# Optimization experiments

Hardware: AMD Instinct MI355X
Metric: run time of the kernel (lower is better)

## Reference

```python
import jax, jax.numpy as jnp
import numpy as np

B, N, K = 2, 1024, 32
NUM_RBF = 16
NUM_POS = 16
EDGE_C = 128
MAXREL = 32
# atoms15 = [N, CA, C, O, virtual-CB, SC0..SC9]; 25 bb-bb pairs + 40 bb-sidechain pairs
_bb = np.arange(5)
SRC = np.concatenate([np.repeat(_bb, 5), np.repeat(np.arange(4), 10)])  # (65,)
DST = np.concatenate([np.tile(_bb, 5), np.tile(np.arange(5, 15), 4)])   # (65,)
P = 65
EDGE_IN = NUM_POS + NUM_RBF * P + 1  # 1057


def setup_inputs() -> dict:
    key = jax.random.key(0)
    ks = jax.random.split(key, 12)
    return {
        "atom14_coords": jax.random.normal(ks[0], (B, N, 14, 3), jnp.float32),
        "atom14_cond_mask": jnp.ones((B, N, 14), jnp.float32),
        "noise": jax.random.normal(ks[1], (B, N, 14, 3), jnp.float32),
        "residue_index": jnp.arange(B * N, dtype=jnp.int32).reshape(B, N),
        "asym_id": jax.random.randint(ks[2], (B, N), 0, 4, jnp.int32),
        "token_bonds": jax.random.uniform(ks[3], (B, N, N), jnp.float32),
        "is_ligand": jax.random.bernoulli(ks[4], 0.2, (B, N)),
        "pos_W": jax.random.normal(ks[5], (2 * MAXREL + 2, NUM_POS), jnp.float32) * 0.1,
        "pos_b": jax.random.normal(ks[6], (NUM_POS,), jnp.float32) * 0.1,
        "edge_W": jax.random.normal(ks[7], (EDGE_IN, EDGE_C), jnp.float32) * 0.02,
        "ln_gamma": jnp.ones((EDGE_C,), jnp.float32),
        "ln_beta": jnp.zeros((EDGE_C,), jnp.float32),
    }


def _gather_nodes(x, idx):
    # x: [B,N,...], idx: [B,N,K] -> [B,N,K,...]
    return jax.vmap(lambda a, i: a[i])(x, idx)


def _rbf(D):
    # D: [...,] -> [..., NUM_RBF]
    D_mu = jnp.linspace(2.0, 22.0, NUM_RBF)
    D_sigma = (22.0 - 2.0) / NUM_RBF
    return jnp.exp(-(((D[..., None] - D_mu) / D_sigma) ** 2))


def reference(atom14_coords, atom14_cond_mask, noise, residue_index, asym_id,
              token_bonds, is_ligand, pos_W, pos_b, edge_W, ln_gamma, ln_beta):
    X = atom14_coords + noise
    X = jnp.where(atom14_cond_mask[..., None] > 0, X, X[..., 1:2, :])
    CA = X[..., 1, :]                                  # [B,N,3]
    mask = atom14_cond_mask[..., 1]                    # [B,N]

    # --- KNN on CA distances ---
    mask_2D = mask[:, None, :] * mask[:, :, None]      # [B,N,N]
    dX = CA[:, None, :, :] - CA[:, :, None, :]
    D = mask_2D * jnp.sqrt(jnp.sum(dX * dX, -1) + 1e-6)
    D_max = jnp.max(D, -1, keepdims=True)
    D_adjust = D + (1.0 - mask_2D) * D_max
    neg_vals, E_idx = jax.lax.top_k(-D_adjust, K)      # smallest K, ascending
    D_neighbors = -neg_vals                            # [B,N,K]

    # --- virtual CB and 15-atom set ---
    b = X[:, :, 1, :] - X[:, :, 0, :]
    c = X[:, :, 2, :] - X[:, :, 1, :]
    a = jnp.cross(b, c)
    Cb = -0.58273431 * a + 0.56802827 * b - 0.54067466 * c + X[:, :, 1, :]
    atoms15 = jnp.concatenate([X[:, :, :4, :], Cb[:, :, None, :], X[:, :, 4:14, :]], axis=2)  # [B,N,15,3]

    # --- fused gather + pairwise distances + RBF over 65 atom pairs ---
    nb_atoms = _gather_nodes(atoms15, E_idx)           # [B,N,K,15,3]
    A = atoms15[:, :, SRC, :]                          # [B,N,65,3]
    Bn = nb_atoms[:, :, :, DST, :]                     # [B,N,K,65,3]
    diff = A[:, :, None, :, :] - Bn
    D_pairs = jnp.sqrt(jnp.sum(diff * diff, -1) + 1e-6)   # [B,N,K,65]
    RBF_all = _rbf(D_pairs).reshape(B, N, K, P * NUM_RBF)  # [B,N,K,1040]

    # --- positional encodings ---
    offset = residue_index[:, :, None] - residue_index[:, None, :]
    offset_nb = jnp.take_along_axis(offset, E_idx, axis=2)     # [B,N,K]
    chain_labels = asym_id  # use_multichain_encoding=True
    d_chains = (chain_labels[:, :, None] == chain_labels[:, None, :]).astype(jnp.int32)
    E_chains = jnp.take_along_axis(d_chains, E_idx, axis=2)    # [B,N,K]
    d = jnp.clip(offset_nb + MAXREL, 0, 2 * MAXREL) * E_chains + (1 - E_chains) * (2 * MAXREL + 1)
    d_onehot = jax.nn.one_hot(d, 2 * MAXREL + 2, dtype=jnp.float32)
    E_positional = d_onehot @ pos_W + pos_b                    # [B,N,K,16]

    # --- token bonds ---
    tb_mask = jnp.logical_or(is_ligand[:, :, None], is_ligand[:, None, :])
    tb = token_bonds * tb_mask.astype(token_bonds.dtype)
    tb_nb = jnp.take_along_axis(tb, E_idx, axis=2)[..., None]  # [B,N,K,1]

    # --- edge embedding + layernorm ---
    E = jnp.concatenate([E_positional, RBF_all, tb_nb], axis=-1)  # [B,N,K,1057]
    E = E @ edge_W                                                # [B,N,K,128]
    mu = jnp.mean(E, -1, keepdims=True)
    var = jnp.mean((E - mu) ** 2, -1, keepdims=True)
    E = (E - mu) / jnp.sqrt(var + 1e-5) * ln_gamma + ln_beta
    return (E, E_idx, D_neighbors)
```

## Files before the change

### kernel.cpp

```cpp
#include <hip/hip_runtime.h>
#include <math.h>

#define BB 2
#define NN 1024
#define KNN 32
#define PP 65
#define NRBF 16
#define EC 128
#define KPAD 1088
#define NCHUNK 17
#define NKT 34

typedef __attribute__((ext_vector_type(8))) short bf16x8;
typedef __attribute__((ext_vector_type(4))) float f32x4;

__device__ __forceinline__ ushort f2bf(float f) {
    union { float f; unsigned u; } v; v.f = f;
    unsigned r = v.u + 0x7fffu + ((v.u >> 16) & 1u);
    return (ushort)(r >> 16);
}

__global__ __launch_bounds__(256) void k_atoms(
    const float* __restrict__ coords, const float* __restrict__ mask,
    const float* __restrict__ noise, float* __restrict__ atoms15)
{
    int idx = blockIdx.x * blockDim.x + threadIdx.x;
    if (idx >= BB * NN) return;
    const float* c  = coords + (size_t)idx * 42;
    const float* nz = noise  + (size_t)idx * 42;
    const float* m  = mask   + (size_t)idx * 14;

    float X[14][3];
    float x1[3];
#pragma unroll
    for (int d = 0; d < 3; d++) x1[d] = c[3 + d] + nz[3 + d];
#pragma unroll
    for (int a = 0; a < 14; a++) {
        bool mm = m[a] > 0.0f;
#pragma unroll
        for (int d = 0; d < 3; d++) {
            float v = c[a * 3 + d] + nz[a * 3 + d];
            X[a][d] = mm ? v : x1[d];
        }
    }
    float bv[3], cv[3], av[3], cb[3];
#pragma unroll
    for (int d = 0; d < 3; d++) { bv[d] = X[1][d] - X[0][d]; cv[d] = X[2][d] - X[1][d]; }
    av[0] = bv[1] * cv[2] - bv[2] * cv[1];
    av[1] = bv[2] * cv[0] - bv[0] * cv[2];
    av[2] = bv[0] * cv[1] - bv[1] * cv[0];
#pragma unroll
    for (int d = 0; d < 3; d++)
        cb[d] = -0.58273431f * av[d] + 0.56802827f * bv[d] - 0.54067466f * cv[d] + X[1][d];

    float* o = atoms15 + (size_t)idx * 45;
#pragma unroll
    for (int a = 0; a < 4; a++)
#pragma unroll
        for (int d = 0; d < 3; d++) o[a * 3 + d] = X[a][d];
#pragma unroll
    for (int d = 0; d < 3; d++) o[4 * 3 + d] = cb[d];
#pragma unroll
    for (int a = 0; a < 10; a++)
#pragma unroll
        for (int d = 0; d < 3; d++) o[(5 + a) * 3 + d] = X[4 + a][d];
}

__global__ __launch_bounds__(256) void k_knn(
    const float* __restrict__ atoms15, const float* __restrict__ cond,
    float* __restrict__ out_idx_f, float* __restrict__ out_d, int* __restrict__ eidx)
{
    __shared__ float Dadj[NN];
    __shared__ float m2s[NN];
    __shared__ float rmax[4];
    __shared__ float candv[128];
    __shared__ int   candj[128];

    int row = blockIdx.x;
    int b = row >> 10, i = row & (NN - 1);
    int t = threadIdx.x;
    int ln = t & 63, wv = t >> 6;
    const float* ab = atoms15 + (size_t)b * NN * 45;
    float cax = ab[(size_t)i * 45 + 3];
    float cay = ab[(size_t)i * 45 + 4];
    float caz = ab[(size_t)i * 45 + 5];
    float mi = cond[(size_t)row * 14 + 1];

    float lmax = -1e30f;
    for (int j = t; j < NN; j += 256) {
        float dx = cax - ab[(size_t)j * 45 + 3];
        float dy = cay - ab[(size_t)j * 45 + 4];
        float dz = caz - ab[(size_t)j * 45 + 5];
        float mj = cond[((size_t)b * NN + j) * 14 + 1];
        float m2 = mi * mj;
        float D = m2 * sqrtf(dx * dx + dy * dy + dz * dz + 1e-6f);
        Dadj[j] = D; m2s[j] = m2;
        lmax = fmaxf(lmax, D);
    }
#pragma unroll
    for (int off = 32; off > 0; off >>= 1) lmax = fmaxf(lmax, __shfl_xor(lmax, off));
    if (ln == 0) rmax[wv] = lmax;
    __syncthreads();
    float Dmax = fmaxf(fmaxf(rmax[0], rmax[1]), fmaxf(rmax[2], rmax[3]));
    for (int j = t; j < NN; j += 256) Dadj[j] += (1.0f - m2s[j]) * Dmax;
    __syncthreads();

    const int base = wv * 256 + ln;
    float v0 = Dadj[base];
    float v1 = Dadj[base + 64];
    float v2 = Dadj[base + 128];
    float v3 = Dadj[base + 192];

    float selv = 0.0f; int seli = 0;
    for (int k = 0; k < KNN; k++) {
        float bv = v0; int bj = base;
        if (v1 < bv) { bv = v1; bj = base + 64;  }
        if (v2 < bv) { bv = v2; bj = base + 128; }
        if (v3 < bv) { bv = v3; bj = base + 192; }
#pragma unroll
        for (int off = 1; off < 64; off <<= 1) {
            float ov = __shfl_xor(bv, off);
            int   oj = __shfl_xor(bj, off);
            if (ov < bv || (ov == bv && oj < bj)) { bv = ov; bj = oj; }
        }
        if (ln == k) { selv = bv; seli = bj; }
        if (bj == base)            v0 = 1e30f;
        else if (bj == base + 64)  v1 = 1e30f;
        else if (bj == base + 128) v2 = 1e30f;
        else if (bj == base + 192) v3 = 1e30f;
    }
    if (ln < KNN) { candv[wv * KNN + ln] = selv; candj[wv * KNN + ln] = seli; }
    __syncthreads();

    if (wv == 0) {
        float c0v = candv[ln];      int c0j = candj[ln];
        float c1v = candv[64 + ln]; int c1j = candj[64 + ln];
        float fv = 0.0f; int fj = 0;
        for (int k = 0; k < KNN; k++) {
            float bv; int bj;
            if (c0v < c1v || (c0v == c1v && c0j < c1j)) { bv = c0v; bj = c0j; }
            else                                        { bv = c1v; bj = c1j; }
#pragma unroll
            for (int off = 1; off < 64; off <<= 1) {
                float ov = __shfl_xor(bv, off);
                int   oj = __shfl_xor(bj, off);
                if (ov < bv || (ov == bv && oj < bj)) { bv = ov; bj = oj; }
            }
            if (ln == k) { fv = bv; fj = bj; }
            if (bj == c0j) c0v = 1e30f;
            if (bj == c1j) c1v = 1e30f;
        }
        if (ln < KNN) {
            size_t o = (size_t)row * KNN + ln;
            out_d[o]     = fv;
            out_idx_f[o] = (float)fj;
            eidx[o]      = fj;
        }
    }
}

__global__ __launch_bounds__(256) void k_wprep(const float* __restrict__ W,
                                               ushort* __restrict__ wf)
{
    int x = blockIdx.x * 256 + threadIdx.x;
    if (x >= NKT * 8 * 64) return;
    int l = x & 63;
    int n16 = (x >> 6) & 7;
    int kt = x >> 9;
    int col = n16 * 16 + (l & 15);
    int kb  = kt * 32 + (l >> 4) * 8;
    ushort v[8];
#pragma unroll
    for (int j = 0; j < 8; j++) {
        int k = kb + j;
        float f = (k < 1057) ? W[(size_t)k * EC + col] : 0.0f;
        v[j] = f2bf(f);
    }
    *(uint4*)&wf[(size_t)x * 8] = *(uint4*)&v[0];
}

__global__ __launch_bounds__(256) void k_edge(
    const float* __restrict__ atoms15, const int* __restrict__ eidx,
    const int* __restrict__ resi, const int* __restrict__ asym,
    const float* __restrict__ tbonds, const int* __restrict__ islig,
    const float* __restrict__ posW, const float* __restrict__ posb,
    const ushort* __restrict__ wfrag, const float* __restrict__ gamma_,
    const float* __restrict__ beta_, float* __restrict__ outE)
{
    __shared__ int   nb[64];
    __shared__ float tbv[64];
    __shared__ float Crow[2][45];
    __shared__ float Brow[64][45];
    __shared__ float epos[64][16];
    __shared__ float Dp[64][PP];
    __shared__ __attribute__((aligned(16))) ushort F[2][64][72];
    __shared__ float part[2][64][2];

    int blk = blockIdx.x;
    int row0 = blk * 2;
    int b = row0 >> 10;
    int t = threadIdx.x;

    if (t < 64) nb[t] = eidx[(size_t)row0 * KNN + t];
    __syncthreads();

    if (t < 90) {
        int e = t / 45, r = t - e * 45;
        Crow[e][r] = atoms15[((size_t)(row0 + e)) * 45 + r];
    }
    {
        int e = t & 63;
        const float* src = atoms15 + ((size_t)(b * NN) + nb[e]) * 45;
#pragma unroll
        for (int q = 0; q < 12; q++) {
            int r = (t >> 6) * 12 + q;
            if (r < 45) Brow[e][r] = src[r];
        }
    }
    for (int x = t; x < 64 * 16; x += 256) {
        int e = x >> 4, r = x & 15;
        int ri = row0 + (e >> 5);
        int ii = ri & (NN - 1);
        int j = nb[e];
        int off = resi[(b << 10) + ii] - resi[(b << 10) + j];
        bool same = (asym[(b << 10) + ii] == asym[(b << 10) + j]);
        int d = same ? min(max(off + 32, 0), 64) : 65;
        epos[e][r] = posW[d * 16 + r] + posb[r];
    }
    if (t < 64) {
        int ri = row0 + (t >> 5);
        int ii = ri & (NN - 1);
        int j = nb[t];
        bool lg = (islig[(b << 10) + ii] != 0) || (islig[(b << 10) + j] != 0);
        tbv[t] = lg ? tbonds[((size_t)((b << 10) + ii)) * NN + j] : 0.0f;
    }
    __syncthreads();

    for (int x = t; x < 64 * PP; x += 256) {
        int e = x / PP, p = x - e * PP;
        int s, dd;
        if (p < 25) { s = p / 5; dd = p - s * 5; }
        else { int q = p - 25; s = q / 10; dd = 5 + (q - s * 10); }
        int cc = e >> 5;
        float dx = Crow[cc][s * 3 + 0] - Brow[e][dd * 3 + 0];
        float dy = Crow[cc][s * 3 + 1] - Brow[e][dd * 3 + 1];
        float dz = Crow[cc][s * 3 + 2] - Brow[e][dd * 3 + 2];
        Dp[e][p] = sqrtf(dx * dx + dy * dy + dz * dz + 1e-6f);
    }
    __syncthreads();

    const int l  = t & 63;
    const int w  = t >> 6;
    const int wm = w >> 1, wn = w & 1;
    const int lc = l & 15, g = l >> 4;

    f32x4 acc[2][4] = {};

    auto STAGE = [&](int cs, int buf) {
        int e = l;
        int fb = w;
        float vals[16];
        if (cs == 0 && fb == 0) {
#pragma unroll
            for (int i2 = 0; i2 < 16; i2++) vals[i2] = epos[e][i2];
        } else if (cs == 16 && fb >= 2) {
#pragma unroll
            for (int i2 = 0; i2 < 16; i2++) vals[i2] = 0.0f;
            if (fb == 2) vals[0] = tbv[e];
        } else {
            int p = 4 * cs + fb - 1;
            float d = Dp[e][p];
#pragma unroll
            for (int i2 = 0; i2 < 16; i2++) {
                float u = (d - (2.0f + (float)i2 * (20.0f / 15.0f))) * 0.8f;
                vals[i2] = __expf(-u * u);
            }
        }
        ushort us[16];
#pragma unroll
        for (int i2 = 0; i2 < 16; i2++) us[i2] = f2bf(vals[i2]);
        *(uint4*)&F[buf][e][fb * 16]     = *(uint4*)&us[0];
        *(uint4*)&F[buf][e][fb * 16 + 8] = *(uint4*)&us[8];
    };

    STAGE(0, 0);
    __syncthreads();

    for (int c = 0; c < NCHUNK; c++) {
        int cur = c & 1;
        if (c + 1 < NCHUNK) STAGE(c + 1, cur ^ 1);

#pragma unroll
        for (int ks = 0; ks < 2; ks++) {
            bf16x8 a0 = *(const bf16x8*)&F[cur][wm * 32 + lc][ks * 32 + 8 * g];
            bf16x8 a1 = *(const bf16x8*)&F[cur][wm * 32 + 16 + lc][ks * 32 + 8 * g];
            int kt = c * 2 + ks;
#pragma unroll
            for (int ni = 0; ni < 4; ni++) {
                bf16x8 bfg = *(const bf16x8*)&wfrag[(((size_t)kt * 8 + wn * 4 + ni) * 64 + l) * 8];
                acc[0][ni] = __builtin_amdgcn_mfma_f32_16x16x32_bf16(a0, bfg, acc[0][ni], 0, 0, 0);
                acc[1][ni] = __builtin_amdgcn_mfma_f32_16x16x32_bf16(a1, bfg, acc[1][ni], 0, 0, 0);
            }
        }
        __syncthreads();
    }

    float gv[4], bev[4];
#pragma unroll
    for (int ni = 0; ni < 4; ni++) {
        int col = wn * 64 + ni * 16 + lc;
        gv[ni]  = gamma_[col];
        bev[ni] = beta_[col];
    }
#pragma unroll
    for (int mi = 0; mi < 2; mi++)
#pragma unroll
        for (int reg = 0; reg < 4; reg++) {
            float s = 0.0f, q = 0.0f;
#pragma unroll
            for (int ni = 0; ni < 4; ni++) {
                float v = acc[mi][ni][reg];
                s += v; q += v * v;
            }
#pragma unroll
            for (int m = 1; m < 16; m <<= 1) {
                s += __shfl_xor(s, m);
                q += __shfl_xor(q, m);
            }
            int srow = wm * 32 + mi * 16 + g * 4 + reg;
            if (lc == 0) { part[wn][srow][0] = s; part[wn][srow][1] = q; }
        }
    __syncthreads();
#pragma unroll
    for (int mi = 0; mi < 2; mi++)
#pragma unroll
        for (int reg = 0; reg < 4; reg++) {
            int srow = wm * 32 + mi * 16 + g * 4 + reg;
            float s = part[0][srow][0] + part[1][srow][0];
            float q = part[0][srow][1] + part[1][srow][1];
            float mu  = s * (1.0f / 128.0f);
            float var = q * (1.0f / 128.0f) - mu * mu;
            float rstd = rsqrtf(var + 1e-5f);
            size_t obase = ((size_t)blk * 64 + srow) * EC;
#pragma unroll
            for (int ni = 0; ni < 4; ni++) {
                float v = (acc[mi][ni][reg] - mu) * rstd * gv[ni] + bev[ni];
                outE[obase + wn * 64 + ni * 16 + lc] = v;
            }
        }
}

extern "C" void kernel_launch(void* const* d_in, const int* in_sizes, int n_in,
                              void* d_out, int out_size, void* d_ws, size_t ws_size,
                              hipStream_t stream)
{
    const float* coords = (const float*)d_in[0];
    const float* cond   = (const float*)d_in[1];
    const float* noise  = (const float*)d_in[2];
    const int*   resi   = (const int*)d_in[3];
    const int*   asym   = (const int*)d_in[4];
    const float* tbonds = (const float*)d_in[5];
    const int*   islig  = (const int*)d_in[6];
    const float* posW   = (const float*)d_in[7];
    const float* posb   = (const float*)d_in[8];
    const float* edgeW  = (const float*)d_in[9];
    const float* gamma_ = (const float*)d_in[10];
    const float* beta_  = (const float*)d_in[11];

    float* outE   = (float*)d_out;
    float* outIdx = outE + (size_t)BB * NN * KNN * EC;
    float* outD   = outIdx + (size_t)BB * NN * KNN;

    float*  atoms15 = (float*)d_ws;
    int*    eidx    = (int*)((char*)d_ws + 368640);
    ushort* wfrag   = (ushort*)((char*)d_ws + 368640 + 262144);

    k_wprep<<<(NKT * 8 * 64 + 255) / 256, 256, 0, stream>>>(edgeW, wfrag);
    k_atoms<<<(BB * NN + 255) / 256, 256, 0, stream>>>(coords, cond, noise, atoms15);
    k_knn<<<BB * NN, 256, 0, stream>>>(atoms15, cond, outIdx, outD, eidx);
    k_edge<<<BB * NN / 2, 256, 0, stream>>>(atoms15, eidx, resi, asym, tbonds, islig,
                                            posW, posb, wfrag, gamma_, beta_, outE);
}
```

Before: 233.8 us.

## Assign one KNN row per wavefront and stage CA coordinates in shared memory

The KNN kernel now processes four rows per block, one per wavefront. Each block stages the batch's CA coordinates and masks in LDS once, and each lane holds 16 distances in registers. This removes the cross-wave candidate merge, the extra syncthreads, and the per-row reload of strided atoms15 data from global memory. In exchange each lane scans 16 register values per selection step, which raises register use and per-iteration ALU work, and the grid shrinks to a quarter of the blocks.

New measurement: 196.8 us. 15.8% less time.

```diff
diff --git a/kernel.cpp b/kernel.cpp
--- a/kernel.cpp
+++ b/kernel.cpp
@@ -70,92 +70,68 @@
     const float* __restrict__ atoms15, const float* __restrict__ cond,
     float* __restrict__ out_idx_f, float* __restrict__ out_d, int* __restrict__ eidx)
 {
-    __shared__ float Dadj[NN];
-    __shared__ float m2s[NN];
-    __shared__ float rmax[4];
-    __shared__ float candv[128];
-    __shared__ int   candj[128];
-
-    int row = blockIdx.x;
-    int b = row >> 10, i = row & (NN - 1);
+    __shared__ float CAx[NN], CAy[NN], CAz[NN], CAw[NN];
+
     int t = threadIdx.x;
-    int ln = t & 63, wv = t >> 6;
-    const float* ab = atoms15 + (size_t)b * NN * 45;
-    float cax = ab[(size_t)i * 45 + 3];
-    float cay = ab[(size_t)i * 45 + 4];
-    float caz = ab[(size_t)i * 45 + 5];
-    float mi = cond[(size_t)row * 14 + 1];
-
+    int ln = t & 63, w = t >> 6;
+    int row0 = blockIdx.x * 4;
+    int b = row0 >> 10;
+
+    for (int j = t; j < NN; j += 256) {
+        const float* aj = atoms15 + ((size_t)b * NN + j) * 45;
+        CAx[j] = aj[3]; CAy[j] = aj[4]; CAz[j] = aj[5];
+        CAw[j] = cond[((size_t)b * NN + j) * 14 + 1];
+    }
+    __syncthreads();
+
+    int row = row0 + w;
+    int i = row & (NN - 1);
+    float mx = CAx[i], my = CAy[i], mz = CAz[i], mi = CAw[i];
+
+    float v[16];
     float lmax = -1e30f;
-    for (int j = t; j < NN; j += 256) {
-        float dx = cax - ab[(size_t)j * 45 + 3];
-        float dy = cay - ab[(size_t)j * 45 + 4];
-        float dz = caz - ab[(size_t)j * 45 + 5];
-        float mj = cond[((size_t)b * NN + j) * 14 + 1];
-        float m2 = mi * mj;
+#pragma unroll
+    for (int q = 0; q < 16; q++) {
+        int j = ln + 64 * q;
+        float dx = mx - CAx[j], dy = my - CAy[j], dz = mz - CAz[j];
+        float m2 = mi * CAw[j];
         float D = m2 * sqrtf(dx * dx + dy * dy + dz * dz + 1e-6f);
-        Dadj[j] = D; m2s[j] = m2;
+        v[q] = D;
         lmax = fmaxf(lmax, D);
     }
 #pragma unroll
     for (int off = 32; off > 0; off >>= 1) lmax = fmaxf(lmax, __shfl_xor(lmax, off));
-    if (ln == 0) rmax[wv] = lmax;
-    __syncthreads();
-    float Dmax = fmaxf(fmaxf(rmax[0], rmax[1]), fmaxf(rmax[2], rmax[3]));
-    for (int j = t; j < NN; j += 256) Dadj[j] += (1.0f - m2s[j]) * Dmax;
-    __syncthreads();
-
-    const int base = wv * 256 + ln;
-    float v0 = Dadj[base];
-    float v1 = Dadj[base + 64];
-    float v2 = Dadj[base + 128];
-    float v3 = Dadj[base + 192];
-
-    float selv = 0.0f; int seli = 0;
+#pragma unroll
+    for (int q = 0; q < 16; q++) {
+        float m2 = mi * CAw[ln + 64 * q];
+        v[q] += (1.0f - m2) * lmax;
+    }
+
+    float selv = 0.0f; int selj = 0;
     for (int k = 0; k < KNN; k++) {
-        float bv = v0; int bj = base;
-        if (v1 < bv) { bv = v1; bj = base + 64;  }
-        if (v2 < bv) { bv = v2; bj = base + 128; }
-        if (v3 < bv) { bv = v3; bj = base + 192; }
+        float bv = v[0]; int bq = 0;
+#pragma unroll
+        for (int q = 1; q < 16; q++) {
+            if (v[q] < bv) { bv = v[q]; bq = q; }
+        }
+        int bj = ln + (bq << 6);
 #pragma unroll
         for (int off = 1; off < 64; off <<= 1) {
             float ov = __shfl_xor(bv, off);
             int   oj = __shfl_xor(bj, off);
             if (ov < bv || (ov == bv && oj < bj)) { bv = ov; bj = oj; }
         }
-        if (ln == k) { selv = bv; seli = bj; }
-        if (bj == base)            v0 = 1e30f;
-        else if (bj == base + 64)  v1 = 1e30f;
-        else if (bj == base + 128) v2 = 1e30f;
-        else if (bj == base + 192) v3 = 1e30f;
-    }
-    if (ln < KNN) { candv[wv * KNN + ln] = selv; candj[wv * KNN + ln] = seli; }
-    __syncthreads();
-
-    if (wv == 0) {
-        float c0v = candv[ln];      int c0j = candj[ln];
-        float c1v = candv[64 + ln]; int c1j = candj[64 + ln];
-        float fv = 0.0f; int fj = 0;
-        for (int k = 0; k < KNN; k++) {
-            float bv; int bj;
-            if (c0v < c1v || (c0v == c1v && c0j < c1j)) { bv = c0v; bj = c0j; }
-            else                                        { bv = c1v; bj = c1j; }
-#pragma unroll
-            for (int off = 1; off < 64; off <<= 1) {
-                float ov = __shfl_xor(bv, off);
-                int   oj = __shfl_xor(bj, off);
-                if (ov < bv || (ov == bv && oj < bj)) { bv = ov; bj = oj; }
-            }
-            if (ln == k) { fv = bv; fj = bj; }
-            if (bj == c0j) c0v = 1e30f;
-            if (bj == c1j) c1v = 1e30f;
-        }
-        if (ln < KNN) {
-            size_t o = (size_t)row * KNN + ln;
-            out_d[o]     = fv;
-            out_idx_f[o] = (float)fj;
-            eidx[o]      = fj;
-        }
+        if (ln == k) { selv = bv; selj = bj; }
+#pragma unroll
+        for (int q = 0; q < 16; q++) {
+            if (bj == ln + (q << 6)) v[q] = 1e30f;
+        }
+    }
+    if (ln < KNN) {
+        size_t o = (size_t)row * KNN + ln;
+        out_d[o]     = selv;
+        out_idx_f[o] = (float)selj;
+        eidx[o]      = selj;
     }
 }
 
@@ -377,7 +353,7 @@
 
     k_wprep<<<(NKT * 8 * 64 + 255) / 256, 256, 0, stream>>>(edgeW, wfrag);
     k_atoms<<<(BB * NN + 255) / 256, 256, 0, stream>>>(coords, cond, noise, atoms15);
-    k_knn<<<BB * NN, 256, 0, stream>>>(atoms15, cond, outIdx, outD, eidx);
+    k_knn<<<BB * NN / 4, 256, 0, stream>>>(atoms15, cond, outIdx, outD, eidx);
     k_edge<<<BB * NN / 2, 256, 0, stream>>>(atoms15, eidx, resi, asym, tbonds, islig,
                                             posW, posb, wfrag, gamma_, beta_, outE);
 }
```
